# Performance work log

Hardware: AMD Instinct MI355X
Metric: run time of the kernel (lower is better)

The kernel has to match this reference:

```python
import jax, jax.numpy as jnp
import numpy as np
import math

B, N, DIN, H, DH, DV, DENC, MAXLEN = 8, 1024, 1024, 8, 128, 64, 32, 1024
EPS = 1e-5


def _make_pe():
    # sinusoidal table, stored as a learnable parameter in the torch module
    pos = np.arange(MAXLEN, dtype=np.float32)[:, None]
    div = np.exp(np.arange(0, DENC, 2, dtype=np.float32) * (-math.log(10000.0) / DENC))
    pe = np.zeros((MAXLEN, DENC), np.float32)
    pe[:, 0::2] = np.sin(pos * div)
    pe[:, 1::2] = np.cos(pos * div)
    return jnp.asarray(pe)[None]  # (1, MAXLEN, DENC)


def setup_inputs() -> dict:
    key = jax.random.key(0)
    ks = jax.random.split(key, 4)
    dq = DH * H  # = d_q = d_k = 1024
    return {
        "x": jax.random.normal(ks[0], (B, N, DIN), jnp.float32),
        "gamma": jnp.ones((1, 1, DIN), jnp.float32),
        "beta": jnp.zeros((1, 1, DIN), jnp.float32),
        "pe": _make_pe(),
        "W_pos": jax.random.normal(ks[1], (DIN + DENC, DIN), jnp.float32) * 0.02,
        "b_pos": jnp.zeros((DIN,), jnp.float32),
        "W_qkv": jax.random.normal(ks[2], (DIN, 2 * dq + DV * H), jnp.float32) * 0.02,
        "b_qkv": jnp.zeros((2 * dq + DV * H,), jnp.float32),
        "W_out": jax.random.normal(ks[3], (DV * H, DIN), jnp.float32) * 0.02,
        "b_out": jnp.zeros((DIN,), jnp.float32),
        "scale": jnp.asarray(1.414, jnp.float32),
    }


def reference(x, gamma, beta, pe, W_pos, b_pos, W_qkv, b_qkv, W_out, b_out, scale):
    Bq, Nq, _ = x.shape
    # PositionalEncoding: concat sinusoidal table, project back to d_in, residual add
    pos_in = jnp.concatenate([x, jnp.broadcast_to(pe[:, :Nq], (Bq, Nq, DENC))], axis=-1)
    h = x + (pos_in @ W_pos + b_pos)
    # FeatureNorm: normalize over the SEQUENCE dim (dim=1), biased variance
    mean = h.mean(axis=1, keepdims=True)
    var = h.var(axis=1, keepdims=True)
    hn = gamma * (h - mean) * jax.lax.rsqrt(var + EPS) + beta
    # QKV projection and head split
    qkv = hn @ W_qkv + b_qkv
    dq = DH * H
    q = qkv[..., :dq].reshape(Bq, Nq, H, DH).transpose(0, 2, 1, 3)       # (B,H,N,DH)
    k = qkv[..., dq:2 * dq].reshape(Bq, Nq, H, DH).transpose(0, 2, 1, 3)  # (B,H,N,DH)
    v = qkv[..., 2 * dq:].reshape(Bq, Nq, H, DV).transpose(0, 2, 1, 3)    # (B,H,N,DV)
    # for_twdit branch: attn = softmax(-(cdist(q,k)/scale)^2) == softmax(-||q-k||^2/scale^2)
    sq = jnp.sum(q * q, axis=-1)  # (B,H,N)
    sk = jnp.sum(k * k, axis=-1)  # (B,H,N)
    d2 = sq[..., :, None] + sk[..., None, :] - 2.0 * jnp.einsum('bhnc,bhmc->bhnm', q, k)
    d2 = jnp.maximum(d2, 0.0)  # cdist is a true (nonnegative) distance
    attn = jax.nn.softmax(-d2 / (scale * scale), axis=-1)  # (B,H,N,N)
    out = jnp.einsum('bhnm,bhmd->bhnd', attn, v)            # (B,H,N,DV)
    out = out.transpose(0, 2, 1, 3).reshape(Bq, Nq, H * DV)
    return x + (out @ W_out + b_out)
```

## Files before the change

kernel.cpp:

```cpp
#include <hip/hip_runtime.h>
#include <math.h>

typedef __bf16 bf16;
typedef __attribute__((ext_vector_type(8))) __bf16 bf16x8;
typedef __attribute__((ext_vector_type(4))) float f32x4;

#define MFMA16(a, b, c) __builtin_amdgcn_mfma_f32_16x16x32_bf16(a, b, c, 0, 0, 0)

__device__ __forceinline__ void gld_lds16(const void* g, void* l) {
  __builtin_amdgcn_global_load_lds(
      (const __attribute__((address_space(1))) unsigned int*)g,
      (__attribute__((address_space(3))) unsigned int*)l, 16, 0, 0);
}

__global__ __launch_bounds__(256) void prep_kernel(
    const float* __restrict__ x, const float* __restrict__ W_pos,
    const float* __restrict__ W_qkv, const float* __restrict__ W_out,
    const float* __restrict__ pe,
    bf16* __restrict__ x_bf, bf16* __restrict__ wpos_p, bf16* __restrict__ wqkv_p,
    bf16* __restrict__ wout_p, bf16* __restrict__ pe_pj) {
  __shared__ float tile[32][33];
  const int tid = threadIdx.x;
  int blk = blockIdx.x;
  if (blk < 4096) {
    int idx = blk * 256 + tid;
    const float4 a = ((const float4*)x)[idx * 2];
    const float4 b = ((const float4*)x)[idx * 2 + 1];
    bf16x8 o = {(bf16)a.x, (bf16)a.y, (bf16)a.z, (bf16)a.w,
                (bf16)b.x, (bf16)b.y, (bf16)b.z, (bf16)b.w};
    *(bf16x8*)(x_bf + (size_t)idx * 8) = o;
    return;
  }
  blk -= 4096;
  if (blk < 4096) {
    const float* W; bf16* BP; int K, N, bx, by;
    if (blk < 1024)      { W = W_pos; BP = wpos_p; K = 1024; N = 1024; bx = blk & 31; by = blk >> 5; }
    else if (blk < 3584) { int b2 = blk - 1024; W = W_qkv; BP = wqkv_p; K = 1024; N = 2560; bx = b2 % 80; by = b2 / 80; }
    else                 { int b2 = blk - 3584; W = W_out; BP = wout_p; K = 512;  N = 1024; bx = b2 & 31; by = b2 >> 5; }
    const int n0 = bx * 32, k0 = by * 32;
    const int tx = tid & 31, ty = tid >> 5;
#pragma unroll
    for (int i = 0; i < 4; ++i)
      tile[ty + 8 * i][tx] = W[(size_t)(k0 + ty + 8 * i) * N + n0 + tx];
    __syncthreads();
    if (tid < 128) {
      int cc = tid & 31, kq = tid >> 5;
      int c = n0 + cc, k = k0 + kq * 8;
      bf16x8 v;
#pragma unroll
      for (int i = 0; i < 8; ++i) v[i] = (bf16)tile[kq * 8 + i][cc];
      *(bf16x8*)(BP + ((size_t)(c >> 4) * (K >> 3) + (k >> 3)) * 128 + (c & 15) * 8) = v;
    }
    return;
  }
  blk -= 4096;
  int idx = blk * 256 + tid;
  int n = idx >> 10, c = idx & 1023;
  float s = 0.f;
#pragma unroll
  for (int e = 0; e < 32; ++e)
    s += pe[n * 32 + e] * W_pos[(size_t)(1024 + e) * 1024 + c];
  pe_pj[idx] = (bf16)s;
}

template <int NT, int OUT_BF16>
__global__ __launch_bounds__(512, 4) void gemm_bd(
    const bf16* __restrict__ A, const bf16* __restrict__ BP, void* __restrict__ Cout,
    int M, int N, int K,
    const float* __restrict__ bias, const bf16* __restrict__ add_full,
    const bf16* __restrict__ add_mod) {
  __shared__ __align__(16) bf16 As[3][128 * 64];
  const int tid = threadIdx.x;
  const int wave = tid >> 6, lane = tid & 63;
  const int wr = wave >> 2, wc = wave & 3;
  const int lr = lane & 15, lg = lane >> 4;
  const int KB = K >> 3;

  const int nwg = gridDim.x * gridDim.y;
  const int bid = blockIdx.y * gridDim.x + blockIdx.x;
  const int s = (bid & 7) * (nwg >> 3) + (bid >> 3);
  const int row0 = (s / gridDim.x) * 128, col0 = (s % gridDim.x) * 256;
  const int cb0 = (col0 >> 4) + wc * 4;

  const int trow = tid >> 3;
  const int cbd = ((tid & 7) * 16) ^ ((trow & 7) << 4);
  const bf16* asrc = A + (size_t)(row0 + trow) * K + (cbd >> 1);
  f32x4 acc[4][4] = {};

  auto STAGE = [&](int sel, int t) {
    char* al = (char*)&As[sel][0] + tid * 16;
    gld_lds16(asrc + t * 64, al);
    gld_lds16(asrc + (size_t)64 * K + t * 64, al + 8192);
  };

  STAGE(0, 0);
  STAGE(1, 1);
  asm volatile("s_waitcnt vmcnt(2)" ::: "memory");
  __builtin_amdgcn_s_barrier();

#pragma unroll
  for (int t = 0; t < NT; ++t) {
    if (t + 2 < NT) STAGE((t + 2) % 3, t + 2);
    const char* Ab = (const char*)&As[t % 3][0];
#pragma unroll
    for (int kc = 0; kc < 2; ++kc) {
      const int kb = (t << 3) + kc * 4 + lg;
      bf16x8 bfr[4], af[4];
#pragma unroll
      for (int nt = 0; nt < 4; ++nt)
        bfr[nt] = *(const bf16x8*)(BP + ((size_t)(cb0 + nt) * KB + kb) * 128 + lr * 8);
#pragma unroll
      for (int mt = 0; mt < 4; ++mt) {
        int r = wr * 64 + mt * 16 + lr;
        af[mt] = *(const bf16x8*)(Ab + r * 128 + ((kc * 64 + lg * 16) ^ ((r & 7) << 4)));
      }
      __builtin_amdgcn_s_setprio(1);
#pragma unroll
      for (int mt = 0; mt < 4; ++mt)
#pragma unroll
        for (int nt = 0; nt < 4; ++nt)
          acc[mt][nt] = MFMA16(af[mt], bfr[nt], acc[mt][nt]);
      __builtin_amdgcn_s_setprio(0);
    }
    if (t + 2 < NT)
      asm volatile("s_waitcnt vmcnt(2)" ::: "memory");
    else
      asm volatile("s_waitcnt vmcnt(0)" ::: "memory");
    __builtin_amdgcn_s_barrier();
  }

#pragma unroll
  for (int mt = 0; mt < 4; ++mt) {
#pragma unroll
    for (int v = 0; v < 4; ++v) {
      int r = row0 + wr * 64 + mt * 16 + lg * 4 + v;
#pragma unroll
      for (int nt = 0; nt < 4; ++nt) {
        int c = col0 + wc * 64 + nt * 16 + lr;
        float val = acc[mt][nt][v];
        if (bias) val += bias[c];
        if (add_full) val += (float)add_full[(size_t)r * N + c];
        if (add_mod) val += (float)add_mod[(size_t)(r & 1023) * N + c];
        if (OUT_BF16)
          ((bf16*)Cout)[(size_t)r * N + c] = (bf16)val;
        else
          ((float*)Cout)[(size_t)r * N + c] = val;
      }
    }
  }
}

__global__ __launch_bounds__(512) void featnorm_kernel(const bf16* __restrict__ h,
                                                       bf16* __restrict__ hn,
                                                       const float* __restrict__ gamma,
                                                       const float* __restrict__ beta) {
  const int b = blockIdx.x >> 4;
  const int d0 = (blockIdx.x & 15) << 6;
  const int tid = threadIdx.x;
  const int c = tid & 63, g = tid >> 6;
  const size_t base = (size_t)b * (1024 * 1024) + d0 + c;
  float s = 0.f, s2 = 0.f;
  for (int n = g * 128; n < g * 128 + 128; ++n) {
    float v = (float)h[base + (size_t)n * 1024];
    s += v; s2 += v * v;
  }
  __shared__ float rs[8][64], rs2[8][64];
  rs[g][c] = s; rs2[g][c] = s2;
  __syncthreads();
  __shared__ float smean[64], srstd[64];
  if (tid < 64) {
    float S = 0.f, S2 = 0.f;
#pragma unroll
    for (int q = 0; q < 8; ++q) { S += rs[q][tid]; S2 += rs2[q][tid]; }
    float mean = S * (1.f / 1024.f);
    float var = S2 * (1.f / 1024.f) - mean * mean;
    smean[tid] = mean;
    srstd[tid] = rsqrtf(var + 1e-5f);
  }
  __syncthreads();
  const float mean = smean[c], rstd = srstd[c];
  const float gm = gamma[d0 + c], bt = beta[d0 + c];
  for (int n = g * 128; n < g * 128 + 128; ++n) {
    size_t idx = base + (size_t)n * 1024;
    hn[idx] = (bf16)(gm * ((float)h[idx] - mean) * rstd + bt);
  }
}

__global__ __launch_bounds__(256) void skvt_kernel(const bf16* __restrict__ qkv,
                                                   const float* __restrict__ scale_ptr,
                                                   float* __restrict__ skl,
                                                   bf16* __restrict__ vT) {
  const int tid = threadIdx.x;
  if (blockIdx.x < 4096) {
    const int lr = tid & 15;
    const int task = blockIdx.x * 16 + (tid >> 4);
    const int bh = task >> 10, n = task & 1023;
    const int b = bh >> 3, h = bh & 7;
    const bf16x8 v = *(const bf16x8*)(qkv + (size_t)(b * 1024 + n) * 2560 +
                                      1024 + h * 128 + lr * 8);
    float s = 0.f;
#pragma unroll
    for (int i = 0; i < 8; ++i) { float f = (float)v[i]; s += f * f; }
#pragma unroll
    for (int off = 1; off < 16; off <<= 1) s += __shfl_xor(s, off);
    if (lr == 0) {
      float sc = scale_ptr[0];
      skl[task] = s * (1.44269504f / (sc * sc));
    }
    return;
  }
  __shared__ bf16 tile[32][34];
  const int blk = blockIdx.x - 4096;
  const int b = blk >> 9;
  const int rem = blk & 511;
  const int c0 = (rem >> 5) * 32, n0 = (rem & 31) * 32;
  const int tx = tid & 31, ty = tid >> 5;
#pragma unroll
  for (int i = 0; i < 4; ++i)
    tile[ty + 8 * i][tx] = qkv[(size_t)(b * 1024 + n0 + ty + 8 * i) * 2560 + 2048 + c0 + tx];
  __syncthreads();
#pragma unroll
  for (int i = 0; i < 4; ++i)
    vT[(size_t)(b * 512 + c0 + ty + 8 * i) * 1024 + n0 + tx] = tile[tx][ty + 8 * i];
}

__global__ __launch_bounds__(512, 4) void attn_mfma(const bf16* __restrict__ qkv,
                                                    const bf16* __restrict__ vT,
                                                    const float* __restrict__ skl,
                                                    const float* __restrict__ scale_ptr,
                                                    bf16* __restrict__ attn_o) {
  const int swz = ((blockIdx.x & 7) << 6) + (blockIdx.x >> 3);
  const int it = swz & 7, bh = swz >> 3;
  const int b = bh >> 3, h = bh & 7;
  const int i0 = it * 128;
  const int tid = threadIdx.x, wave = tid >> 6, lane = tid & 63;
  const int lr = lane & 15, lg = lane >> 4;
  const float sc = scale_ptr[0];
  const float c2 = 2.f * 1.44269504f / (sc * sc);

  __shared__ __align__(16) bf16 Ks[2][64 * 128];
  __shared__ __align__(16) bf16 Vs[2][64 * 64];
  __shared__ __align__(16) bf16 Ps[8][16 * 64];
  __shared__ float sks[1024];

  const int trowK = tid >> 4;
  const int cbKd = ((tid & 15) * 16) ^ ((trowK & 7) << 4);
  const bf16* ksrc = qkv + (size_t)(b * 1024 + trowK) * 2560 + 1024 + h * 128 + (cbKd >> 1);
  const int trowV = tid >> 3;
  const int cbVd = ((tid & 7) * 16) ^ ((trowV & 7) << 4);
  const bf16* vsrc = vT + (size_t)(b * 512 + h * 64 + trowV) * 1024 + (cbVd >> 1);

  auto STAGE = [&](int sel, int jt) {
    const bf16* kp = ksrc + (size_t)jt * 64 * 2560;
    char* kl = (char*)&Ks[sel][0] + tid * 16;
    gld_lds16(kp, kl);
    gld_lds16(kp + (size_t)32 * 2560, kl + 8192);
    gld_lds16(vsrc + jt * 64, (char*)&Vs[sel][0] + tid * 16);
  };

  {
    float2 sv = ((const float2*)(skl + (size_t)bh * 1024))[tid];
    *(float2*)&sks[tid * 2] = sv;
  }
  bf16x8 qf[4];
  {
    const bf16* qrow = qkv + (size_t)(b * 1024 + i0 + wave * 16 + lr) * 2560 + h * 128;
#pragma unroll
    for (int kc = 0; kc < 4; ++kc) qf[kc] = *(const bf16x8*)(qrow + kc * 32 + lg * 8);
  }
  __syncthreads();

  bf16x8 vones;
  {
    bf16 one_or_zero = (lr == 0) ? (bf16)1.0f : (bf16)0.0f;
#pragma unroll
    for (int i = 0; i < 8; ++i) vones[i] = one_or_zero;
  }

  f32x4 o[4] = {};
  f32x4 o_l = {};

  STAGE(0, 0);
  asm volatile("s_waitcnt vmcnt(0)" ::: "memory");
  __builtin_amdgcn_s_barrier();

#pragma unroll
  for (int jt = 0; jt < 16; ++jt) {
    const int cur = jt & 1;
    if (jt < 15) STAGE(cur ^ 1, jt + 1);

    f32x4 sacc[4] = {};
    __builtin_amdgcn_s_setprio(1);
#pragma unroll
    for (int kc = 0; kc < 4; ++kc) {
#pragma unroll
      for (int nt = 0; nt < 4; ++nt) {
        int j = nt * 16 + lr;
        int byte = j * 256 + (((kc * 32 + lg * 8) * 2) ^ ((j & 7) << 4));
        bf16x8 kf = *(const bf16x8*)((const char*)&Ks[cur][0] + byte);
        sacc[nt] = MFMA16(qf[kc], kf, sacc[nt]);
      }
    }
    __builtin_amdgcn_s_setprio(0);

#pragma unroll
    for (int nt = 0; nt < 4; ++nt) {
      float skv = sks[jt * 64 + nt * 16 + lr];
#pragma unroll
      for (int v = 0; v < 4; ++v) {
        float p = __builtin_amdgcn_exp2f(sacc[nt][v] * c2 - skv);
        int r = lg * 4 + v, c = nt * 16 + lr;
        int byte = r * 128 + ((c * 2) ^ ((r & 7) << 4));
        *(bf16*)((char*)&Ps[wave][0] + byte) = (bf16)p;
      }
    }
    bf16x8 pf[2];
#pragma unroll
    for (int kc = 0; kc < 2; ++kc) {
      int byte = lr * 128 + (((kc * 32 + lg * 8) * 2) ^ ((lr & 7) << 4));
      pf[kc] = *(const bf16x8*)((const char*)&Ps[wave][0] + byte);
    }
    __builtin_amdgcn_s_setprio(1);
#pragma unroll
    for (int kc = 0; kc < 2; ++kc) {
#pragma unroll
      for (int nt = 0; nt < 4; ++nt) {
        int d = nt * 16 + lr;
        int byte = d * 128 + (((kc * 32 + lg * 8) * 2) ^ ((d & 7) << 4));
        bf16x8 vf = *(const bf16x8*)((const char*)&Vs[cur][0] + byte);
        o[nt] = MFMA16(pf[kc], vf, o[nt]);
      }
      o_l = MFMA16(pf[kc], vones, o_l);
    }
    __builtin_amdgcn_s_setprio(0);

    asm volatile("s_waitcnt vmcnt(0)" ::: "memory");
    __builtin_amdgcn_s_barrier();
  }

#pragma unroll
  for (int v = 0; v < 4; ++v) {
    float ls = __shfl(o_l[v], lg << 4);
    float inv = 1.f / ls;
    int r = i0 + wave * 16 + lg * 4 + v;
#pragma unroll
    for (int nt = 0; nt < 4; ++nt) {
      int c = h * 64 + nt * 16 + lr;
      attn_o[(size_t)(b * 1024 + r) * 512 + c] = (bf16)(o[nt][v] * inv);
    }
  }
}

extern "C" void kernel_launch(void* const* d_in, const int* in_sizes, int n_in,
                              void* d_out, int out_size, void* d_ws, size_t ws_size,
                              hipStream_t stream) {
  const float* x     = (const float*)d_in[0];
  const float* gamma = (const float*)d_in[1];
  const float* beta  = (const float*)d_in[2];
  const float* pe    = (const float*)d_in[3];
  const float* W_pos = (const float*)d_in[4];
  const float* b_pos = (const float*)d_in[5];
  const float* W_qkv = (const float*)d_in[6];
  const float* b_qkv = (const float*)d_in[7];
  const float* W_out = (const float*)d_in[8];
  const float* b_out = (const float*)d_in[9];
  const float* scale = (const float*)d_in[10];
  float* outp = (float*)d_out;

  char* ws = (char*)d_ws;
  const size_t MB = 1 << 20;
  bf16* x_bf   = (bf16*)(ws);
  bf16* wpos_p = (bf16*)(ws + 16 * MB);
  bf16* wqkv_p = (bf16*)(ws + 18 * MB);
  bf16* wout_p = (bf16*)(ws + 23 * MB);
  bf16* pe_pj  = (bf16*)(ws + 24 * MB);
  bf16* vT     = (bf16*)(ws + 24 * MB);
  bf16* h      = (bf16*)(ws + 32 * MB);
  bf16* attn_o = (bf16*)(ws + 32 * MB);
  bf16* qkv    = (bf16*)(ws + 48 * MB);
  float* skl   = (float*)(ws + 88 * MB);
  bf16* hn     = (bf16*)(ws + 96 * MB);

  prep_kernel<<<12288, 256, 0, stream>>>(x, W_pos, W_qkv, W_out, pe,
                                         x_bf, wpos_p, wqkv_p, wout_p, pe_pj);
  gemm_bd<16, 1><<<dim3(4, 64), 512, 0, stream>>>(x_bf, wpos_p, h, 8192, 1024, 1024,
                                                  b_pos, x_bf, pe_pj);
  featnorm_kernel<<<128, 512, 0, stream>>>(h, hn, gamma, beta);
  gemm_bd<16, 1><<<dim3(10, 64), 512, 0, stream>>>(hn, wqkv_p, qkv, 8192, 2560, 1024,
                                                   b_qkv, nullptr, nullptr);
  skvt_kernel<<<8192, 256, 0, stream>>>(qkv, scale, skl, vT);
  attn_mfma<<<512, 512, 0, stream>>>(qkv, vT, skl, scale, attn_o);
  gemm_bd<8, 0><<<dim3(4, 64), 512, 0, stream>>>(attn_o, wout_p, outp, 8192, 1024, 512,
                                                 b_out, x_bf, nullptr);
}
```

Measured before the change: 246.3 us.

## Add 4-wave GEMM with larger per-wave tiles for QKV projection

Adds a new GEMM kernel using 256 threads (4 waves), each wave computing a 64x128 output sub-tile with 32 accumulators. A is staged through a triple-buffered swizzled LDS ring, and B is read directly from the pre-packed global weight layout. Launch bounds allow 2 blocks per CU, and workgroup IDs are remapped for locality. The QKV projection now uses this kernel in place of the 8-wave version, aiming for more MFMA work per loaded fragment. The cost is higher register pressure, which may reduce occupancy.

Result: slower. 313.6 us (+27.3%).

```diff
diff --git a/kernel.cpp b/kernel.cpp
--- a/kernel.cpp
+++ b/kernel.cpp
@@ -150,6 +150,94 @@
   }
 }
 
+template <int NT, int OUT_BF16>
+__global__ __launch_bounds__(256, 2) void gemm_w(
+    const bf16* __restrict__ A, const bf16* __restrict__ BP, void* __restrict__ Cout,
+    int M, int N, int K,
+    const float* __restrict__ bias, const bf16* __restrict__ add_full,
+    const bf16* __restrict__ add_mod) {
+  __shared__ __align__(16) bf16 As[3][128 * 64];
+  const int tid = threadIdx.x;
+  const int wave = tid >> 6, lane = tid & 63;
+  const int wr = wave >> 1, wc = wave & 1;
+  const int lr = lane & 15, lg = lane >> 4;
+  const int KB = K >> 3;
+
+  const int nwg = gridDim.x * gridDim.y;
+  const int bid = blockIdx.y * gridDim.x + blockIdx.x;
+  const int s = (bid & 7) * (nwg >> 3) + (bid >> 3);
+  const int row0 = (s / gridDim.x) * 128, col0 = (s % gridDim.x) * 256;
+  const int cb0 = (col0 >> 4) + wc * 8;
+
+  const int trow = tid >> 3;
+  const int cbd = ((tid & 7) * 16) ^ ((trow & 7) << 4);
+  const bf16* asrc = A + (size_t)(row0 + trow) * K + (cbd >> 1);
+  f32x4 acc[4][8] = {};
+
+  auto STAGE = [&](int sel, int t) {
+    char* al = (char*)&As[sel][0] + tid * 16;
+#pragma unroll
+    for (int c = 0; c < 4; ++c)
+      gld_lds16(asrc + (size_t)c * 32 * K + t * 64, al + c * 4096);
+  };
+
+  STAGE(0, 0);
+  STAGE(1, 1);
+  asm volatile("s_waitcnt vmcnt(4)" ::: "memory");
+  __builtin_amdgcn_s_barrier();
+
+#pragma unroll
+  for (int t = 0; t < NT; ++t) {
+    if (t + 2 < NT) STAGE((t + 2) % 3, t + 2);
+    const char* Ab = (const char*)&As[t % 3][0];
+#pragma unroll
+    for (int kc = 0; kc < 2; ++kc) {
+      const int kb = (t << 3) + kc * 4 + lg;
+      bf16x8 bfr[8], af[4];
+#pragma unroll
+      for (int nt = 0; nt < 8; ++nt)
+        bfr[nt] = *(const bf16x8*)(BP + ((size_t)(cb0 + nt) * KB + kb) * 128 + lr * 8);
+#pragma unroll
+      for (int mt = 0; mt < 4; ++mt) {
+        int r = wr * 64 + mt * 16 + lr;
+        af[mt] = *(const bf16x8*)(Ab + r * 128 + ((kc * 64 + lg * 16) ^ ((r & 7) << 4)));
+      }
+      __builtin_amdgcn_s_setprio(1);
+#pragma unroll
+      for (int mt = 0; mt < 4; ++mt)
+#pragma unroll
+        for (int nt = 0; nt < 8; ++nt)
+          acc[mt][nt] = MFMA16(af[mt], bfr[nt], acc[mt][nt]);
+      __builtin_amdgcn_s_setprio(0);
+    }
+    if (t + 2 < NT)
+      asm volatile("s_waitcnt vmcnt(4)" ::: "memory");
+    else
+      asm volatile("s_waitcnt vmcnt(0)" ::: "memory");
+    __builtin_amdgcn_s_barrier();
+  }
+
+#pragma unroll
+  for (int mt = 0; mt < 4; ++mt) {
+#pragma unroll
+    for (int v = 0; v < 4; ++v) {
+      int r = row0 + wr * 64 + mt * 16 + lg * 4 + v;
+#pragma unroll
+      for (int nt = 0; nt < 8; ++nt) {
+        int c = col0 + wc * 128 + nt * 16 + lr;
+        float val = acc[mt][nt][v];
+        if (bias) val += bias[c];
+        if (add_full) val += (float)add_full[(size_t)r * N + c];
+        if (add_mod) val += (float)add_mod[(size_t)(r & 1023) * N + c];
+        if (OUT_BF16)
+          ((bf16*)Cout)[(size_t)r * N + c] = (bf16)val;
+        else
+          ((float*)Cout)[(size_t)r * N + c] = val;
+      }
+    }
+  }
+}
+
 __global__ __launch_bounds__(512) void featnorm_kernel(const bf16* __restrict__ h,
                                                        bf16* __restrict__ hn,
                                                        const float* __restrict__ gamma,
@@ -386,8 +474,8 @@
   gemm_bd<16, 1><<<dim3(4, 64), 512, 0, stream>>>(x_bf, wpos_p, h, 8192, 1024, 1024,
                                                   b_pos, x_bf, pe_pj);
   featnorm_kernel<<<128, 512, 0, stream>>>(h, hn, gamma, beta);
-  gemm_bd<16, 1><<<dim3(10, 64), 512, 0, stream>>>(hn, wqkv_p, qkv, 8192, 2560, 1024,
-                                                   b_qkv, nullptr, nullptr);
+  gemm_w<16, 1><<<dim3(10, 64), 256, 0, stream>>>(hn, wqkv_p, qkv, 8192, 2560, 1024,
+                                                  b_qkv, nullptr, nullptr);
   skvt_kernel<<<8192, 256, 0, stream>>>(qkv, scale, skl, vT);
   attn_mfma<<<512, 512, 0, stream>>>(qkv, vT, skl, scale, attn_o);
   gemm_bd<8, 0><<<dim3(4, 64), 512, 0, stream>>>(attn_o, wout_p, outp, 8192, 1024, 512,
```
